# Optimization experiments

Measured on AMD Instinct MI355X. Metric: run time of the kernel, lower is better.

## Reference

```python
import jax, jax.numpy as jnp
import numpy as np

R = 59        # num relations (58 + 1)
D = 128       # node_feat_size
K = 16        # neighbors_sample


def _lstm(windows, Wk, Wr, b):
    # windows: [N, T, F]; standard Keras LSTM (gate order i, f, g, o).
    N = windows.shape[0]
    z_in = jnp.einsum('ntf,fh->nth', windows, Wk) + b        # [N, T, 4D]
    z_in = jnp.swapaxes(z_in, 0, 1)                          # [T, N, 4D]

    def step(carry, zt):
        h, c = carry
        z = zt + h @ Wr
        i, f, g, o = jnp.split(z, 4, axis=-1)
        i = jax.nn.sigmoid(i)
        f = jax.nn.sigmoid(f)
        g = jnp.tanh(g)
        o = jax.nn.sigmoid(o)
        c = f * c + i * g
        h = o * jnp.tanh(c)
        return (h, c), None

    h0 = jnp.zeros((N, D), windows.dtype)
    (h, _), _ = jax.lax.scan(step, (h0, h0), z_in)
    return h                                                 # [N, D]


def setup_inputs() -> dict:
    key = jax.random.key(0)
    ks = jax.random.split(key, 12)
    N, T, F = 1024, 32, 10
    s = 0.05
    return {
        'windows': jax.random.normal(ks[0], (N, T, F), jnp.float32),
        'neighbors': jax.random.randint(ks[1], (R, N, K), 0, N + 1, jnp.int32),
        'lstm_kernel': jax.random.normal(ks[2], (F, 4 * D), jnp.float32) * s,
        'lstm_recurrent': jax.random.normal(ks[3], (D, 4 * D), jnp.float32) * s,
        'lstm_bias': jax.random.normal(ks[4], (4 * D,), jnp.float32) * s,
        'W_state': jax.random.normal(ks[5], (R, 2 * D + R), jnp.float32) * s,
        'b_state': jax.random.normal(ks[6], (R,), jnp.float32) * s,
        'W_relattn': jax.random.normal(ks[7], (2 * D + R,), jnp.float32) * s,
        'b_relattn': jax.random.normal(ks[8], (1,), jnp.float32) * s,
        'W_pred': jax.random.normal(ks[9], (D, 3), jnp.float32) * s,
        'b_pred': jax.random.normal(ks[10], (3,), jnp.float32) * s,
    }


def reference(windows, neighbors, lstm_kernel, lstm_recurrent, lstm_bias,
              W_state, b_state, W_relattn, b_relattn, W_pred, b_pred):
    cur = _lstm(windows, lstm_kernel, lstm_recurrent, lstm_bias)    # [N, D]
    feats = jnp.concatenate([jnp.zeros((1, D), cur.dtype), cur], 0)  # [N+1, D]

    # --- per-relation state attention ---
    # Dense(1) on concat(cur, nbr, onehot(rel)) splits into three dot products.
    Wc = W_state[:, :D]            # [R, D]
    Wn = W_state[:, D:2 * D]       # [R, D]
    Wrr = W_state[:, 2 * D:]       # [R, R]; onehot picks the diagonal
    rel_term = jnp.diagonal(Wrr) + b_state                  # [R]
    cur_term = cur @ Wc.T                                    # [N, R]
    nbr_proj = feats @ Wn.T                                  # [N+1, R]
    # gather the scalar neighbor projection per relation: [R, N, K]
    nbr_term = jax.vmap(lambda idx, p: p[idx])(neighbors, nbr_proj.T)
    scores = jax.nn.relu(cur_term.T[:, :, None] + nbr_term
                         + rel_term[:, None, None])          # [R, N, K]
    w = jax.nn.softmax(scores, axis=-1)
    nbr_feats = feats[neighbors]                             # [R, N, K, D]
    rel_reps = jnp.einsum('rnk,rnkd->rnd', w, nbr_feats)     # [R, N, D]

    # --- relation attention ---
    wc = W_relattn[:D]
    wn = W_relattn[D:2 * D]
    wr = W_relattn[2 * D:]                                   # [R]
    s2 = jax.nn.relu((cur @ wc)[None, :]
                     + jnp.einsum('rnd,d->rn', rel_reps, wn)
                     + wr[:, None] + b_relattn[0])           # [R, N]
    aw = jax.nn.softmax(s2, axis=0)
    rel_agg = jnp.einsum('rn,rnd->nd', aw, rel_reps)         # [N, D]
    updated = cur + rel_agg

    logits = updated @ W_pred + b_pred                       # [N, 3]
    predictions = jax.nn.softmax(logits, axis=-1)
    return logits, predictions, updated
```

## Files before the change

kernel.cpp:

```cpp
#include <hip/hip_runtime.h>
#include <hip/hip_bf16.h>

constexpr int R  = 59;
constexpr int D  = 128;
constexpr int NK = 16;
constexpr int N  = 1024;
constexpr int T  = 32;
constexpr int F  = 10;
constexpr int H4 = 512;
constexpr int WSTRIDE = 2*D + R;

typedef __attribute__((ext_vector_type(8))) short short8;
typedef __attribute__((ext_vector_type(4))) float f32x4;

__device__ __forceinline__ float sigm(float x) {
  return __builtin_amdgcn_rcpf(1.0f + __expf(-x));
}
__device__ __forceinline__ float tanh_(float x) {
  return 2.0f * __builtin_amdgcn_rcpf(1.0f + __expf(-2.0f * x)) - 1.0f;
}
__device__ __forceinline__ ushort f2bf(float f) {
  unsigned u = __float_as_uint(f);
  u += 0x7FFF + ((u >> 16) & 1);
  return (ushort)(u >> 16);
}
__device__ __forceinline__ float bf2f(ushort u) {
  return __uint_as_float(((unsigned)u) << 16);
}

__device__ int g_detect_f32(const void* windows) {
  const __hip_bfloat16* p = (const __hip_bfloat16*)windows;
  int weird = 0;
  for (int i = 0; i < 128; ++i) {
    float v = __bfloat162float(p[i]);
    float a = fabsf(v);
    if (!(a <= 100.0f) || (v != 0.0f && a < 1e-8f)) ++weird;
  }
  return weird > 8;
}

__device__ __forceinline__ float rdsrc(const void* p, int i, int isf32) {
  return isf32 ? ((const float*)p)[i]
               : __bfloat162float(((const __hip_bfloat16*)p)[i]);
}

struct CvtA {
  const void* small[6];
  int soff[7];
  const void* win;
  const void* wk;
  const void* wr;
  const void* bias;
};

__global__ __launch_bounds__(256) void convert_kernel(
    CvtA a, float* __restrict__ csm, float* __restrict__ wt,
    ushort* __restrict__ bpk, int* __restrict__ flag_out)
{
  __shared__ int sflag;
  if (threadIdx.x == 0) sflag = g_detect_f32(a.win);
  __syncthreads();
  const int isf32 = sflag;
  if (blockIdx.x == 0 && threadIdx.x == 0) flag_out[0] = isf32;
  const int gid = blockIdx.x * 256 + threadIdx.x;
  const int stride = gridDim.x * 256;

  for (int i = gid; i < a.soff[6]; i += stride) {
    int t = 0;
    while (t < 5 && i >= a.soff[t + 1]) ++t;
    csm[i] = rdsrc(a.small[t], i - a.soff[t], isf32);
  }
  for (int i = gid; i < 128 * 128; i += stride) {
    const int d = i >> 7, j = i & 127;
    float v = 0.0f;
    if (j < 59)        v = rdsrc(a.small[0], j * WSTRIDE + D + d, isf32);
    else if (j < 118)  v = rdsrc(a.small[0], (j - 59) * WSTRIDE + d, isf32);
    else if (j == 118) v = rdsrc(a.small[2], d, isf32);
    wt[i] = v;
  }
  for (int fi = gid; fi < 10240; fi += stride) {
    const int l  = fi & 63;
    const int kf = (fi >> 6) % 5;
    const int g  = ((fi >> 6) / 5) & 3;
    const int w  = (fi >> 6) / 20;
    const int col = g * 128 + w * 16 + (l & 15);
    const int q   = l >> 4;
#pragma unroll
    for (int j = 0; j < 8; ++j) {
      const int k = q * 8 + j;
      float v;
      if (kf < 4)      v = rdsrc(a.wr, (kf * 32 + k) * H4 + col, isf32);
      else if (k < 10) v = rdsrc(a.wk, k * H4 + col, isf32);
      else if (k == 10) v = rdsrc(a.bias, col, isf32);
      else             v = 0.0f;
      bpk[fi * 8 + j] = f2bf(v);
    }
  }
}

__global__ __launch_bounds__(512)
__attribute__((amdgpu_waves_per_eu(2, 2)))
void lstm_kernel(const ushort* __restrict__ bpk, const void* __restrict__ win_raw,
                 const int* __restrict__ flagp,
                 float* __restrict__ feats, ushort* __restrict__ fb16)
{
  const int tid = threadIdx.x;
  const int w   = tid >> 6;
  const int l   = tid & 63;
  const int n0  = blockIdx.x * 16;

  __shared__ ushort hbuf[2][16 * 136];
  __shared__ ushort xfrag[T * 64 * 8];

  if (blockIdx.x == 0 && tid < D) { feats[tid] = 0.0f; fb16[tid] = 0; }

  const int isf32 = flagp[0];
  for (int p = tid; p < T * 64; p += 512) {
    const int t = p >> 6, ll = p & 63, s = ll & 15, q = ll >> 4;
    short8 pk;
#pragma unroll
    for (int j = 0; j < 8; ++j) {
      const int f = q * 8 + j;
      float v = (f < F) ? rdsrc(win_raw, (n0 + s) * (T * F) + t * F + f, isf32)
                        : (f == 10 ? 1.0f : 0.0f);
      pk[j] = (short)f2bf(v);
    }
    *(short8*)&xfrag[p * 8] = pk;
  }
  for (int i = tid; i < 2 * 16 * 136; i += 512) ((ushort*)hbuf)[i] = 0;

  short8 B[4][5];
#pragma unroll
  for (int g = 0; g < 4; ++g)
#pragma unroll
    for (int kf = 0; kf < 5; ++kf)
      B[g][kf] = *(const short8*)&bpk[((((w * 4 + g) * 5 + kf) * 64) + l) * 8];

  f32x4 c4 = {0.f, 0.f, 0.f, 0.f};
  float hreg[4];
  const int lq    = l >> 4;
  const int krow0 = lq * 8;
  const int srow0 = lq * 4;
  const int col_d = w * 16 + (l & 15);

  __syncthreads();

  for (int t = 0; t < T; ++t) {
    const ushort* hb = hbuf[t & 1];
    short8 A[5];
#pragma unroll
    for (int kf = 0; kf < 4; ++kf)
      A[kf] = *(const short8*)(hb + (l & 15) * 136 + kf * 32 + krow0);
    A[4] = *(const short8*)(xfrag + (t * 64 + l) * 8);

    f32x4 acc[4];
#pragma unroll
    for (int g = 0; g < 4; ++g) {
      acc[g] = (f32x4){0.f, 0.f, 0.f, 0.f};
#pragma unroll
      for (int kf = 0; kf < 5; ++kf)
        acc[g] = __builtin_amdgcn_mfma_f32_16x16x32_bf16(A[kf], B[g][kf], acc[g], 0, 0, 0);
    }

    ushort* hw = hbuf[(t + 1) & 1];
#pragma unroll
    for (int r = 0; r < 4; ++r) {
      const float i_ = sigm(acc[0][r]);
      const float f_ = sigm(acc[1][r]);
      const float g_ = tanh_(acc[2][r]);
      const float o_ = sigm(acc[3][r]);
      c4[r]   = f_ * c4[r] + i_ * g_;
      hreg[r] = o_ * tanh_(c4[r]);
      hw[(srow0 + r) * 136 + col_d] = f2bf(hreg[r]);
    }
    __syncthreads();
  }

#pragma unroll
  for (int r = 0; r < 4; ++r) {
    feats[(n0 + srow0 + r + 1) * D + col_d] = hreg[r];
    fb16 [(n0 + srow0 + r + 1) * D + col_d] = f2bf(hreg[r]);
  }
}

__global__ __launch_bounds__(128) void proj_kernel(
    const float* __restrict__ feats, const float* __restrict__ wt,
    float* __restrict__ cur_term, float* __restrict__ nbr_proj,
    float* __restrict__ curwc)
{
  const int m = blockIdx.x;
  const int j = threadIdx.x;
  __shared__ float frow[128];
  frow[j] = feats[m * D + j];
  __syncthreads();

  float acc = 0.0f;
#pragma unroll 8
  for (int d = 0; d < 128; ++d)
    acc = fmaf(frow[d], wt[d * 128 + j], acc);

  if (j < 59) nbr_proj[m * R + j] = acc;
  else if (m >= 1) {
    if (j < 118)       cur_term[(m - 1) * R + (j - 59)] = acc;
    else if (j == 118) curwc[m - 1] = acc;
  }
}

__device__ __forceinline__ void store_out(void* out, int i, float v, int outf32) {
  if (outf32) ((float*)out)[i] = v;
  else        ((__hip_bfloat16*)out)[i] = __float2bfloat16(v);
}

__global__ __launch_bounds__(256) void attn_kernel(
    const float* __restrict__ feats, const ushort* __restrict__ fb16,
    const int* __restrict__ neighbors,
    const float* __restrict__ W_state, const float* __restrict__ b_state,
    const float* __restrict__ W_relattn, const float* __restrict__ b_relattn,
    const float* __restrict__ W_pred, const float* __restrict__ b_pred,
    const float* __restrict__ cur_term, const float* __restrict__ nbr_proj,
    const float* __restrict__ curwc, const int* __restrict__ flagp,
    void* __restrict__ out)
{
  const int n   = blockIdx.x;
  const int tid = threadIdx.x;

  __shared__ ushort rr[R * 136];
  __shared__ int    idx_lds[R * NK];
  __shared__ float  w_lds[NK * 60];
  __shared__ float  s2part[16 * 68];
  __shared__ float  wn_lds[D];
  __shared__ float  ct_lds[R];
  __shared__ float  rt_lds[R];
  __shared__ float  s2_lds[R];
  __shared__ float  aw_lds[R];
  __shared__ float  upd_lds[D];
  __shared__ int    sflag;

  if (tid == 0) sflag = flagp[0];
  if (tid < R) {
    ct_lds[tid] = cur_term[n * R + tid];
    rt_lds[tid] = W_state[tid * WSTRIDE + 2 * D + tid] + b_state[tid];
  }
  if (tid >= 128 && tid < 256) wn_lds[tid - 128] = W_relattn[D + (tid - 128)];
  for (int i = tid; i < R * NK; i += 256) {
    const int r = i >> 4, k = i & 15;
    idx_lds[i] = neighbors[(r * N + n) * NK + k];
  }
  __syncthreads();
  const int outf32 = sflag;

  for (int i = tid; i < R * NK; i += 256) {
    const int r = i >> 4, k = i & 15;
    float s = ct_lds[r] + nbr_proj[idx_lds[i] * R + r] + rt_lds[r];
    w_lds[k * 60 + r] = fmaxf(s, 0.0f);
  }
  __syncthreads();

  if (tid < R) {
    float mx = 0.0f;
#pragma unroll
    for (int k = 0; k < NK; ++k) mx = fmaxf(mx, w_lds[k * 60 + tid]);
    float sum = 0.0f;
    float e[NK];
#pragma unroll
    for (int k = 0; k < NK; ++k) {
      e[k] = __expf(w_lds[k * 60 + tid] - mx);
      sum += e[k];
    }
    const float inv = __builtin_amdgcn_rcpf(sum);
#pragma unroll
    for (int k = 0; k < NK; ++k) w_lds[k * 60 + tid] = e[k] * inv;
  }
  __syncthreads();

  {
    const int d8 = tid & 15;
    const int rp = tid >> 4;
    for (int r = rp; r < R; r += 16) {
      float acc[8];
#pragma unroll
      for (int j = 0; j < 8; ++j) acc[j] = 0.0f;
#pragma unroll
      for (int k = 0; k < NK; ++k) {
        const int m = idx_lds[r * NK + k];
        const uint4 v = *(const uint4*)&fb16[m * D + d8 * 8];
        const float wv = w_lds[k * 60 + r];
        acc[0] = fmaf(wv, __uint_as_float(v.x << 16),          acc[0]);
        acc[1] = fmaf(wv, __uint_as_float(v.x & 0xffff0000u),  acc[1]);
        acc[2] = fmaf(wv, __uint_as_float(v.y << 16),          acc[2]);
        acc[3] = fmaf(wv, __uint_as_float(v.y & 0xffff0000u),  acc[3]);
        acc[4] = fmaf(wv, __uint_as_float(v.z << 16),          acc[4]);
        acc[5] = fmaf(wv, __uint_as_float(v.z & 0xffff0000u),  acc[5]);
        acc[6] = fmaf(wv, __uint_as_float(v.w << 16),          acc[6]);
        acc[7] = fmaf(wv, __uint_as_float(v.w & 0xffff0000u),  acc[7]);
      }
      short8 pk;
#pragma unroll
      for (int j = 0; j < 8; ++j) pk[j] = (short)f2bf(acc[j]);
      *(short8*)&rr[r * 136 + d8 * 8] = pk;
      float p = 0.0f;
#pragma unroll
      for (int j = 0; j < 8; ++j) p = fmaf(acc[j], wn_lds[d8 * 8 + j], p);
      s2part[d8 * 68 + r] = p;
    }
  }
  __syncthreads();

  if (tid < R) {
    float dot = 0.0f;
#pragma unroll
    for (int q = 0; q < 16; ++q) dot += s2part[q * 68 + tid];
    float v = curwc[n] + dot + W_relattn[2 * D + tid] + b_relattn[0];
    s2_lds[tid] = fmaxf(v, 0.0f);
  }
  __syncthreads();

  if (tid < 64) {
    float v = (tid < R) ? s2_lds[tid] : -1e30f;
    float mx = v;
    for (int off = 32; off; off >>= 1) mx = fmaxf(mx, __shfl_xor(mx, off));
    float e = (tid < R) ? __expf(v - mx) : 0.0f;
    float sum = e;
    for (int off = 32; off; off >>= 1) sum += __shfl_xor(sum, off);
    if (tid < R) aw_lds[tid] = e / sum;
  }
  __syncthreads();

  if (tid < D) {
    float agg = 0.0f;
    for (int r = 0; r < R; ++r) agg = fmaf(aw_lds[r], bf2f(rr[r * 136 + tid]), agg);
    const float upd = feats[(n + 1) * D + tid] + agg;
    store_out(out, 2 * 3 * N + n * D + tid, upd, outf32);
    upd_lds[tid] = upd;
  }
  __syncthreads();

  if (tid < 64) {
    float p[3];
#pragma unroll
    for (int j = 0; j < 3; ++j) {
      float v = upd_lds[tid] * W_pred[tid * 3 + j] +
                upd_lds[tid + 64] * W_pred[(tid + 64) * 3 + j];
      for (int off = 32; off; off >>= 1) v += __shfl_xor(v, off);
      p[j] = v + b_pred[j];
    }
    if (tid == 0) {
      const float mx = fmaxf(p[0], fmaxf(p[1], p[2]));
      const float e0 = __expf(p[0] - mx), e1 = __expf(p[1] - mx), e2 = __expf(p[2] - mx);
      const float s = e0 + e1 + e2;
      store_out(out, n * 3 + 0, p[0], outf32);
      store_out(out, n * 3 + 1, p[1], outf32);
      store_out(out, n * 3 + 2, p[2], outf32);
      store_out(out, 3 * N + n * 3 + 0, e0 / s, outf32);
      store_out(out, 3 * N + n * 3 + 1, e1 / s, outf32);
      store_out(out, 3 * N + n * 3 + 2, e2 / s, outf32);
    }
  }
}

extern "C" void kernel_launch(void* const* d_in, const int* in_sizes, int n_in,
                              void* d_out, int out_size, void* d_ws, size_t ws_size,
                              hipStream_t stream)
{
  const int* neighbors = (const int*)d_in[1];
  float* ws = (float*)d_ws;

  CvtA ca;
  {
    constexpr int SS[6] = {18585, 59, 315, 1, 384, 3};
    int off = 0;
    for (int i = 0; i < 6; ++i) { ca.small[i] = d_in[5 + i]; ca.soff[i] = off; off += SS[i]; }
    ca.soff[6] = off;
    ca.win  = d_in[0];
    ca.wk   = d_in[2];
    ca.wr   = d_in[3];
    ca.bias = d_in[4];
  }

  float*  csm      = ws;
  float*  wtpack   = csm + 19360;
  float*  feats    = wtpack + 16384;
  float*  cur_term = feats + 131200;
  float*  nbr_proj = cur_term + 60416;
  float*  curwc    = nbr_proj + 60480;
  int*    flagp    = (int*)(curwc + 1024);
  ushort* bpk      = (ushort*)(curwc + 1040);
  ushort* fb16     = bpk + 81920;

  const float* c_Wstate = csm;
  const float* c_bstate = csm + 18585;
  const float* c_Wrel   = csm + 18644;
  const float* c_brel   = csm + 18959;
  const float* c_Wpred  = csm + 18960;
  const float* c_bpred  = csm + 19344;

  convert_kernel<<<256, 256, 0, stream>>>(ca, csm, wtpack, bpk, flagp);
  lstm_kernel<<<N / 16, 512, 0, stream>>>(bpk, d_in[0], flagp, feats, fb16);
  proj_kernel<<<N + 1, 128, 0, stream>>>(feats, wtpack, cur_term, nbr_proj, curwc);
  attn_kernel<<<N, 256, 0, stream>>>(feats, fb16, neighbors, c_Wstate, c_bstate, c_Wrel,
                                     c_brel, c_Wpred, c_bpred,
                                     cur_term, nbr_proj, curwc, flagp, d_out);
}
```

Baseline: 75.22 us.

## Process two independent 16-row groups per LSTM block to interleave MFMA chains

```diff
diff --git a/kernel.cpp b/kernel.cpp
--- a/kernel.cpp
+++ b/kernel.cpp
@@ -107,27 +107,34 @@
   const int tid = threadIdx.x;
   const int w   = tid >> 6;
   const int l   = tid & 63;
-  const int n0  = blockIdx.x * 16;
-
-  __shared__ ushort hbuf[2][16 * 136];
-  __shared__ ushort xfrag[T * 64 * 8];
+  const int n0  = blockIdx.x * 32;
+
+  __shared__ ushort hbufA[2][16 * 136];
+  __shared__ ushort hbufB[2][16 * 136];
+  __shared__ ushort xfragA[T * 64 * 8];
+  __shared__ ushort xfragB[T * 64 * 8];
 
   if (blockIdx.x == 0 && tid < D) { feats[tid] = 0.0f; fb16[tid] = 0; }
 
   const int isf32 = flagp[0];
-  for (int p = tid; p < T * 64; p += 512) {
-    const int t = p >> 6, ll = p & 63, s = ll & 15, q = ll >> 4;
+  for (int p = tid; p < 2 * T * 64; p += 512) {
+    const int grp = p >> 11;
+    const int pp  = p & 2047;
+    const int t = pp >> 6, ll = pp & 63, s = ll & 15, q = ll >> 4;
     short8 pk;
 #pragma unroll
     for (int j = 0; j < 8; ++j) {
       const int f = q * 8 + j;
-      float v = (f < F) ? rdsrc(win_raw, (n0 + s) * (T * F) + t * F + f, isf32)
+      float v = (f < F) ? rdsrc(win_raw, (n0 + grp * 16 + s) * (T * F) + t * F + f, isf32)
                         : (f == 10 ? 1.0f : 0.0f);
       pk[j] = (short)f2bf(v);
     }
-    *(short8*)&xfrag[p * 8] = pk;
-  }
-  for (int i = tid; i < 2 * 16 * 136; i += 512) ((ushort*)hbuf)[i] = 0;
+    *(short8*)&(grp ? xfragB : xfragA)[pp * 8] = pk;
+  }
+  for (int i = tid; i < 2 * 16 * 136; i += 512) {
+    ((ushort*)hbufA)[i] = 0;
+    ((ushort*)hbufB)[i] = 0;
+  }
 
   short8 B[4][5];
 #pragma unroll
@@ -136,50 +143,70 @@
     for (int kf = 0; kf < 5; ++kf)
       B[g][kf] = *(const short8*)&bpk[((((w * 4 + g) * 5 + kf) * 64) + l) * 8];
 
-  f32x4 c4 = {0.f, 0.f, 0.f, 0.f};
-  float hreg[4];
+  f32x4 c4A = {0.f, 0.f, 0.f, 0.f}, c4B = {0.f, 0.f, 0.f, 0.f};
+  float hregA[4], hregB[4];
   const int lq    = l >> 4;
   const int krow0 = lq * 8;
   const int srow0 = lq * 4;
   const int col_d = w * 16 + (l & 15);
+  const int abase = (l & 15) * 136;
 
   __syncthreads();
 
   for (int t = 0; t < T; ++t) {
-    const ushort* hb = hbuf[t & 1];
-    short8 A[5];
-#pragma unroll
-    for (int kf = 0; kf < 4; ++kf)
-      A[kf] = *(const short8*)(hb + (l & 15) * 136 + kf * 32 + krow0);
-    A[4] = *(const short8*)(xfrag + (t * 64 + l) * 8);
-
-    f32x4 acc[4];
+    const ushort* hA = hbufA[t & 1];
+    const ushort* hB = hbufB[t & 1];
+    short8 Aa[5], Ab[5];
+#pragma unroll
+    for (int kf = 0; kf < 4; ++kf) {
+      Aa[kf] = *(const short8*)(hA + abase + kf * 32 + krow0);
+      Ab[kf] = *(const short8*)(hB + abase + kf * 32 + krow0);
+    }
+    Aa[4] = *(const short8*)(xfragA + (t * 64 + l) * 8);
+    Ab[4] = *(const short8*)(xfragB + (t * 64 + l) * 8);
+
+    f32x4 aA[4], aB[4];
 #pragma unroll
     for (int g = 0; g < 4; ++g) {
-      acc[g] = (f32x4){0.f, 0.f, 0.f, 0.f};
-#pragma unroll
-      for (int kf = 0; kf < 5; ++kf)
-        acc[g] = __builtin_amdgcn_mfma_f32_16x16x32_bf16(A[kf], B[g][kf], acc[g], 0, 0, 0);
-    }
-
-    ushort* hw = hbuf[(t + 1) & 1];
+      aA[g] = (f32x4){0.f, 0.f, 0.f, 0.f};
+      aB[g] = (f32x4){0.f, 0.f, 0.f, 0.f};
+    }
+#pragma unroll
+    for (int kf = 0; kf < 5; ++kf)
+#pragma unroll
+      for (int g = 0; g < 4; ++g) {
+        aA[g] = __builtin_amdgcn_mfma_f32_16x16x32_bf16(Aa[kf], B[g][kf], aA[g], 0, 0, 0);
+        aB[g] = __builtin_amdgcn_mfma_f32_16x16x32_bf16(Ab[kf], B[g][kf], aB[g], 0, 0, 0);
+      }
+
+    ushort* wA = hbufA[(t + 1) & 1];
+    ushort* wB = hbufB[(t + 1) & 1];
 #pragma unroll
     for (int r = 0; r < 4; ++r) {
-      const float i_ = sigm(acc[0][r]);
-      const float f_ = sigm(acc[1][r]);
-      const float g_ = tanh_(acc[2][r]);
-      const float o_ = sigm(acc[3][r]);
-      c4[r]   = f_ * c4[r] + i_ * g_;
-      hreg[r] = o_ * tanh_(c4[r]);
-      hw[(srow0 + r) * 136 + col_d] = f2bf(hreg[r]);
+      const float iA = sigm(aA[0][r]);
+      const float fA = sigm(aA[1][r]);
+      const float gA = tanh_(aA[2][r]);
+      const float oA = sigm(aA[3][r]);
+      c4A[r]   = fA * c4A[r] + iA * gA;
+      hregA[r] = oA * tanh_(c4A[r]);
+      wA[(srow0 + r) * 136 + col_d] = f2bf(hregA[r]);
+      const float iB = sigm(aB[0][r]);
+      const float fB = sigm(aB[1][r]);
+      const float gB = tanh_(aB[2][r]);
+      const float oB = sigm(aB[3][r]);
+      c4B[r]   = fB * c4B[r] + iB * gB;
+      hregB[r] = oB * tanh_(c4B[r]);
+      wB[(srow0 + r) * 136 + col_d] = f2bf(hregB[r]);
     }
     __syncthreads();
   }
 
 #pragma unroll
   for (int r = 0; r < 4; ++r) {
-    feats[(n0 + srow0 + r + 1) * D + col_d] = hreg[r];
-    fb16 [(n0 + srow0 + r + 1) * D + col_d] = f2bf(hreg[r]);
+    feats[(n0 + srow0 + r + 1) * D + col_d]      = hregA[r];
+    fb16 [(n0 + srow0 + r + 1) * D + col_d]      = f2bf(hregA[r]);
+    feats[(n0 + 16 + srow0 + r + 1) * D + col_d] = hregB[r];
+    fb16 [(n0 + 16 + srow0 + r + 1) * D + col_d] = f2bf(hregB[r]);
   }
 }
 
@@ -395,7 +422,7 @@
   const float* c_bpred  = csm + 19344;
 
   convert_kernel<<<256, 256, 0, stream>>>(ca, csm, wtpack, bpk, flagp);
-  lstm_kernel<<<N / 16, 512, 0, stream>>>(bpk, d_in[0], flagp, feats, fb16);
+  lstm_kernel<<<N / 32, 512, 0, stream>>>(bpk, d_in[0], flagp, feats, fb16);
   proj_kernel<<<N + 1, 128, 0, stream>>>(feats, wtpack, cur_term, nbr_proj, curwc);
   attn_kernel<<<N, 256, 0, stream>>>(feats, fb16, neighbors, c_Wstate, c_bstate, c_Wrel,
                                      c_brel, c_Wpred, c_bpred,
```

Result: slower. 103.7 us (+37.8%).
